# Kernel tuning notes

Measured on AMD Instinct MI355X. Metric: run time of the kernel, lower is better.

Reference implementation:

```python
import jax, jax.numpy as jnp
import numpy as np

FEATURE_MAPS = [38, 19, 10, 5, 3, 1]
NUM_ANCHORS = [4, 6, 6, 6, 4, 4]
SCALES = (0.2, 0.9)
RATIOS = np.array([1.0, 1.0, 2.0, 3.0, 0.5, 1.0 / 3.0])
BACKGROUND_ID = 0
EPS = 1e-6


def _generate_anchors():
    """Replicates AnchorManager._generate_anchors: order is (i, j, k)."""
    all_anchors = []
    for size, n in zip(FEATURE_MAPS, NUM_ANCHORS):
        scales = np.linspace(SCALES[0], SCALES[1], n)
        ratios = RATIOS[:n]
        rs = np.sqrt(ratios)
        w = scales * rs          # [n]
        h = scales / rs          # [n]
        cy = (np.arange(size) + 0.5) / size  # i -> rows (varies slowest)
        cx = (np.arange(size) + 0.5) / size  # j -> cols
        grid = np.zeros((size, size, n, 4), dtype=np.float64)
        grid[..., 0] = cx[None, :, None]
        grid[..., 1] = cy[:, None, None]
        grid[..., 2] = w[None, None, :]
        grid[..., 3] = h[None, None, :]
        all_anchors.append(grid.reshape(-1, 4))
    return np.concatenate(all_anchors).astype(np.float32)  # [A, 4] cxcywh


def _cxcywh_to_xyxy(b):
    cxy, wh = b[..., :2], b[..., 2:]
    return jnp.concatenate([cxy - wh / 2, cxy + wh / 2], axis=-1)


def _xyxy_to_cxcywh(b):
    xy1, xy2 = b[..., :2], b[..., 2:]
    return jnp.concatenate([(xy1 + xy2) / 2, xy2 - xy1], axis=-1)


def setup_inputs() -> dict:
    key = jax.random.key(0)
    k1, k2, k3 = jax.random.split(key, 3)
    B, N = 64, 100
    # valid normalized xyxy gt boxes
    xy = jax.random.uniform(k1, (B, N, 2), dtype=jnp.float32) * 0.8
    wh = jax.random.uniform(k2, (B, N, 2), dtype=jnp.float32) * 0.19 + 0.01
    gt_boxes = jnp.concatenate([xy, xy + wh], axis=-1)
    gt_labels = jax.random.randint(k3, (B, N), 1, 81, dtype=jnp.int64 if jax.config.jax_enable_x64 else jnp.int32).astype(jnp.int32)
    anchors_cxcywh = jnp.asarray(_generate_anchors())          # [A, 4]
    anchors_xyxy = _cxcywh_to_xyxy(anchors_cxcywh)             # [A, 4]
    return {
        "gt_labels": gt_labels,
        "gt_boxes": gt_boxes,
        "anchors_cxcywh": anchors_cxcywh,
        "anchors_xyxy": anchors_xyxy,
    }


def _iou(anchors_xyxy, gt_boxes):
    # anchors_xyxy: [A,4], gt_boxes: [B,N,4] -> iou [B,A,N]
    a = anchors_xyxy[None, :, None, :]   # [1,A,1,4]
    g = gt_boxes[:, None, :, :]          # [B,1,N,4]
    lt = jnp.maximum(a[..., :2], g[..., :2])
    rb = jnp.minimum(a[..., 2:], g[..., 2:])
    wh = jnp.clip(rb - lt, 0.0)
    inter = wh[..., 0] * wh[..., 1]
    area_a = (a[..., 2] - a[..., 0]) * (a[..., 3] - a[..., 1])
    area_g = (g[..., 2] - g[..., 0]) * (g[..., 3] - g[..., 1])
    return (inter / (area_a + area_g - inter)).astype(jnp.float32)


def reference(gt_labels, gt_boxes, anchors_cxcywh, anchors_xyxy):
    B, N = gt_boxes.shape[0], gt_boxes.shape[1]
    A = anchors_cxcywh.shape[0]

    gt_boxes_coco = _xyxy_to_cxcywh(gt_boxes)                  # [B,N,4]
    ious = _iou(anchors_xyxy, gt_boxes)                        # [B,A,N]

    anchors_gt = jnp.max(ious, axis=-1)                        # [B,A]
    anchors_gt_idx = jnp.argmax(ious, axis=-1)                 # [B,A]
    gt_anchors_idx = jnp.argmax(ious, axis=-2)                 # [B,N] best anchor per gt

    # force-match: each gt claims its best anchor
    b_idx = jnp.arange(B)[:, None]
    range_n = jnp.broadcast_to(jnp.arange(N), (B, N))
    anchors_gt_idx = anchors_gt_idx.at[b_idx, gt_anchors_idx].set(range_n)
    anchors_gt = anchors_gt.at[b_idx, gt_anchors_idx].set(2.0)

    pos_mask = anchors_gt > 0.5                                # [B,A]

    matched_gtb = jnp.take_along_axis(gt_boxes_coco, anchors_gt_idx[..., None], axis=1)  # [B,A,4]
    matched_labels = jnp.take_along_axis(gt_labels, anchors_gt_idx, axis=1)              # [B,A]
    encoded_labels = jnp.where(pos_mask, matched_labels, BACKGROUND_ID)

    anc = anchors_cxcywh[None]                                 # [1,A,4]
    enc_cxy = (matched_gtb[..., :2] - anc[..., :2]) / anc[..., 2:]
    enc_wh = jnp.log((matched_gtb[..., 2:] + EPS) / (anc[..., 2:] + EPS))
    encoded = jnp.concatenate([enc_cxy, enc_wh], axis=-1)      # [B,A,4]

    return encoded_labels, encoded, pos_mask
```

## Files before the change

### kernel.cpp

```cpp
#include <hip/hip_runtime.h>
#include <math.h>

#pragma clang fp contract(off)


#define AA 8732
#define NN 100
#define BB 64
#define EPS_F 1e-6f
#define OVR_FLAG 0x10000
#define DEFL 0.9999995f

__constant__ int FM_SIZE[6] = {38, 19, 10, 5, 3, 1};
__constant__ int FM_NF[6]   = {4, 6, 6, 6, 4, 4};
__constant__ int FM_OFF[6]  = {0, 5776, 7942, 8542, 8692, 8728};

__device__ __forceinline__ void geom(const float4 axy, const float4 g,
                                     float area_a, float ag,
                                     float& inter, float& uni) {
    float ltx = fmaxf(axy.x, g.x);
    float lty = fmaxf(axy.y, g.y);
    float rbx = fminf(axy.z, g.z);
    float rby = fminf(axy.w, g.w);
    float w = fmaxf(rbx - ltx, 0.0f);
    float h = fmaxf(rby - lty, 0.0f);
    inter = w * h;
    uni = area_a + ag - inter;
}

template <int N0, int N1>
__device__ __forceinline__ void phaseA(const float4 axy, float area_a,
                                       bool valid,
                                       const float4* sg, const float* sarea,
                                       const float* scurf,
                                       float& am, unsigned& rm, unsigned& cm) {
    #pragma unroll 4
    for (int n = N0; n < N1; n++) {
        float inter, uni;
        geom(axy, sg[n], area_a, sarea[n], inter, uni);
        float qa = inter * __builtin_amdgcn_rcpf(uni);
        bool r = (qa > 0.0f) && (qa >= am * DEFL);
        bool c = valid && (qa >= scurf[n]);
        am = fmaxf(am, qa);
        rm |= (r ? 1u : 0u) << (n - N0);
        cm |= (c ? 1u : 0u) << (n - N0);
    }
}

__global__ __launch_bounds__(256) void iou_pass_kernel(
        const float4* __restrict__ gt_boxes,
        const float4* __restrict__ anchors_xyxy,
        unsigned long long* __restrict__ colmax,
        float* __restrict__ out_val,
        int* __restrict__ out_slot)
{
    const int b = blockIdx.y;
    const int tid = threadIdx.x;
    const int a = blockIdx.x * 256 + tid;
    const bool valid = (a < AA);
    const int ac = valid ? a : (AA - 1);

    __shared__ float4 sg[NN];
    __shared__ float  sarea[NN];
    __shared__ float  scurf[NN];

    if (tid < NN) {
        float4 g = gt_boxes[b * NN + tid];
        sg[tid] = g;
        float ag = (g.z - g.x) * (g.w - g.y);
        sarea[tid] = ag;
        float cx = (g.x + g.z) * 0.5f;
        float cy = (g.y + g.w) * 0.5f;
        float best = 0.0f;
        for (int f = 0; f < 6; f++) {
            int s = FM_SIZE[f];
            int j = (int)(cx * (float)s); j = j < s - 1 ? j : s - 1;
            int i = (int)(cy * (float)s); i = i < s - 1 ? i : s - 1;
            int base = FM_OFF[f] + (i * s + j) * FM_NF[f];
            for (int k = 0; k < FM_NF[f]; k++) {
                float4 an = anchors_xyxy[base + k];
                float area_a = (an.z - an.x) * (an.w - an.y);
                float inter, uni;
                geom(an, g, area_a, ag, inter, uni);
                best = fmaxf(best, inter * __builtin_amdgcn_rcpf(uni));
            }
        }
        scurf[tid] = best * DEFL;
    }
    __syncthreads();

    const float4 axy = anchors_xyxy[ac];
    const float area_a = (axy.z - axy.x) * (axy.w - axy.y);

    float am = 0.0f;
    unsigned rm0 = 0, rm1 = 0, rm2 = 0, rm3 = 0;
    unsigned cm0 = 0, cm1 = 0, cm2 = 0, cm3 = 0;
    phaseA<0, 32>(axy, area_a, valid, sg, sarea, scurf, am, rm0, cm0);
    phaseA<32, 64>(axy, area_a, valid, sg, sarea, scurf, am, rm1, cm1);
    phaseA<64, 96>(axy, area_a, valid, sg, sarea, scurf, am, rm2, cm2);
    phaseA<96, NN>(axy, area_a, valid, sg, sarea, scurf, am, rm3, cm3);

    const float amthr = am * DEFL;
    float bv = 0.0f;
    int bi = 0;
    {
        unsigned rms[4] = {rm0, rm1, rm2, rm3};
        #pragma unroll
        for (int h = 0; h < 4; h++) {
            unsigned m = rms[h];
            const int nb = h * 32;
            while (m) {
                int n = __builtin_ctz(m) + nb;
                m &= m - 1;
                float inter, uni;
                geom(axy, sg[n], area_a, sarea[n], inter, uni);
                float qa = inter * __builtin_amdgcn_rcpf(uni);
                if (qa > 0.0f && qa >= amthr) {
                    float iou = inter / uni;
                    if (iou > bv) { bv = iou; bi = n; }
                }
            }
        }
    }

    {
        unsigned cms[4] = {cm0, cm1, cm2, cm3};
        #pragma unroll
        for (int h = 0; h < 4; h++) {
            unsigned wc = cms[h];
            #pragma unroll
            for (int off = 32; off > 0; off >>= 1)
                wc |= __shfl_xor(wc, off);
            const int nb = h * 32;
            while (wc) {
                int n = __builtin_ctz(wc) + nb;
                wc &= wc - 1;
                float inter, uni;
                geom(axy, sg[n], area_a, sarea[n], inter, uni);
                float qa = inter * __builtin_amdgcn_rcpf(uni);
                bool cc = valid && (qa >= scurf[n]);
                if (__any((int)cc)) {
                    float iou = inter / uni;
                    unsigned qb = cc ? __float_as_uint(iou) : 0u;
                    unsigned mm = qb;
                    #pragma unroll
                    for (int off = 32; off > 0; off >>= 1) {
                        unsigned o = __shfl_xor(mm, off);
                        mm = o > mm ? o : mm;
                    }
                    unsigned long long ball =
                        __ballot((int)(qb == mm && mm > 0u));
                    if (ball) {
                        int leader = __ffsll((long long)ball) - 1;
                        if ((tid & 63) == leader) {
                            unsigned long long v =
                                (((unsigned long long)mm) << 32) |
                                (unsigned long long)(unsigned)(AA - a);
                            atomicMax(colmax + b * NN + n, v);
                            atomicMax((unsigned*)&scurf[n],
                                __float_as_uint(__uint_as_float(mm) * DEFL));
                        }
                    }
                }
            }
        }
    }

    if (valid) {
        const size_t base = (size_t)b * AA + a;
        out_val[base] = bv;
        out_slot[base] = bi;
    }
}

__global__ void scatter_kernel(const unsigned long long* __restrict__ colmax,
                               int* __restrict__ out_slot) {
    const int b = blockIdx.x;
    const int n = threadIdx.x;
    if (n < NN) {
        unsigned long long v = colmax[b * NN + n];
        unsigned low = (unsigned)(v & 0xFFFFFFFFull);
        if (low >= 1u && low <= (unsigned)AA) {
            int idx = AA - (int)low;
            atomicMax(&out_slot[(size_t)b * AA + idx], OVR_FLAG + n);
        }
    }
}

__global__ __launch_bounds__(256) void encode_kernel(
        const int* __restrict__ gt_labels,
        const float4* __restrict__ gt_boxes,
        const float4* __restrict__ anchors_cxcywh,
        float* __restrict__ out)
{
    const int b = blockIdx.y;
    const int tid = threadIdx.x;
    const int a = blockIdx.x * 256 + tid;

    __shared__ float4 sg[NN];
    __shared__ int    slab[NN];
    if (tid < NN) {
        sg[tid]   = gt_boxes[b * NN + tid];
        slab[tid] = gt_labels[b * NN + tid];
    }
    __syncthreads();
    if (a >= AA) return;

    const size_t BA = (size_t)BB * AA;
    const size_t base = (size_t)b * AA + a;

    float bv = out[base];
    int s = ((const int*)(out + 5 * BA))[base];

    int idx; float val;
    if (s >= OVR_FLAG) { idx = s - OVR_FLAG; val = 2.0f; }
    else               { idx = s;            val = bv;   }
    const bool pos = val > 0.5f;

    const float4 g = sg[idx];
    const float gcx = (g.x + g.z) * 0.5f;
    const float gcy = (g.y + g.w) * 0.5f;
    const float gw  = g.z - g.x;
    const float gh  = g.w - g.y;

    const float4 anc = anchors_cxcywh[a];
    const float ecx = (gcx - anc.x) / anc.z;
    const float ecy = (gcy - anc.y) / anc.w;
    const float ew  = logf((gw + EPS_F) / (anc.z + EPS_F));
    const float eh  = logf((gh + EPS_F) / (anc.w + EPS_F));

    out[base] = pos ? (float)slab[idx] : 0.0f;
    ((float4*)(out + BA))[base] = make_float4(ecx, ecy, ew, eh);
    out[5 * BA + base] = pos ? 1.0f : 0.0f;
}

extern "C" void kernel_launch(void* const* d_in, const int* in_sizes, int n_in,
                              void* d_out, int out_size, void* d_ws, size_t ws_size,
                              hipStream_t stream) {
    const int*    gt_labels    = (const int*)d_in[0];
    const float4* gt_boxes     = (const float4*)d_in[1];
    const float4* anchors_cxcy = (const float4*)d_in[2];
    const float4* anchors_xyxy = (const float4*)d_in[3];
    float* out = (float*)d_out;

    const size_t BA = (size_t)BB * AA;
    unsigned long long* colmax = (unsigned long long*)(out + BA);
    int* slot = (int*)(out + 5 * BA);

    (void)hipMemsetAsync(colmax, 0,
                         (size_t)BB * NN * sizeof(unsigned long long), stream);

    dim3 grid((AA + 255) / 256, BB);
    iou_pass_kernel<<<grid, 256, 0, stream>>>(gt_boxes, anchors_xyxy, colmax,
                                              out, slot);
    scatter_kernel<<<BB, 128, 0, stream>>>(colmax, slot);
    encode_kernel<<<grid, 256, 0, stream>>>(gt_labels, gt_boxes, anchors_cxcy,
                                            out);
}
```

Measured before the change: 145.5 us.

## Process two anchors per thread and fuse column-max detection into main IoU loop

Each thread now handles two anchors, so every shared-memory ground-truth load is reused twice. The column-max update moves inline into the main loop through a 64-bit wave max reduction, which removes the second pass that recomputed IoU from per-thread column masks. The per-gt prior best-IoU computation moves to a separate small kernel that also initializes colmax, replacing the memset and the redundant per-block prior work. The trade-off is an extra launch, higher register pressure, half as many blocks, and an __any check on every iteration.

```diff
diff --git a/kernel.cpp b/kernel.cpp
--- a/kernel.cpp
+++ b/kernel.cpp
@@ -28,37 +28,129 @@
     uni = area_a + ag - inter;
 }
 
+__global__ void prior_kernel(const float4* __restrict__ gt_boxes,
+                             const float4* __restrict__ anchors_xyxy,
+                             float* __restrict__ prior,
+                             unsigned long long* __restrict__ colmax) {
+    const int b = blockIdx.x;
+    const int n = threadIdx.x;
+    if (n >= NN) return;
+    float4 g = gt_boxes[b * NN + n];
+    float ag = (g.z - g.x) * (g.w - g.y);
+    float cx = (g.x + g.z) * 0.5f;
+    float cy = (g.y + g.w) * 0.5f;
+    float best = 0.0f;
+    for (int f = 0; f < 6; f++) {
+        int s = FM_SIZE[f];
+        int j = (int)(cx * (float)s); j = j < s - 1 ? j : s - 1;
+        int i = (int)(cy * (float)s); i = i < s - 1 ? i : s - 1;
+        int base = FM_OFF[f] + (i * s + j) * FM_NF[f];
+        for (int k = 0; k < FM_NF[f]; k++) {
+            float4 an = anchors_xyxy[base + k];
+            float area_a = (an.z - an.x) * (an.w - an.y);
+            float inter, uni;
+            geom(an, g, area_a, ag, inter, uni);
+            best = fmaxf(best, inter * __builtin_amdgcn_rcpf(uni));
+        }
+    }
+    float defl = best * DEFL;
+    prior[b * NN + n] = defl;
+    colmax[b * NN + n] = ((unsigned long long)__float_as_uint(defl)) << 32;
+}
+
 template <int N0, int N1>
-__device__ __forceinline__ void phaseA(const float4 axy, float area_a,
-                                       bool valid,
-                                       const float4* sg, const float* sarea,
-                                       const float* scurf,
-                                       float& am, unsigned& rm, unsigned& cm) {
+__device__ __forceinline__ void passChunk(
+        const float4 x0, const float4 x1,
+        const float ar0, const float ar1,
+        const bool v0, const bool v1,
+        const int a0, const int a1,
+        const int b, const int tid,
+        const float4* __restrict__ sg,
+        const float* __restrict__ sarea,
+        float* scurf,
+        unsigned long long* __restrict__ colmax,
+        float& am0, float& am1,
+        unsigned& rm0, unsigned& rm1)
+{
     #pragma unroll 4
     for (int n = N0; n < N1; n++) {
-        float inter, uni;
-        geom(axy, sg[n], area_a, sarea[n], inter, uni);
-        float qa = inter * __builtin_amdgcn_rcpf(uni);
-        bool r = (qa > 0.0f) && (qa >= am * DEFL);
-        bool c = valid && (qa >= scurf[n]);
-        am = fmaxf(am, qa);
-        rm |= (r ? 1u : 0u) << (n - N0);
-        cm |= (c ? 1u : 0u) << (n - N0);
+        float4 g = sg[n];
+        float ag = sarea[n];
+        float i0, u0, i1, u1;
+        geom(x0, g, ar0, ag, i0, u0);
+        geom(x1, g, ar1, ag, i1, u1);
+        float q0 = i0 * __builtin_amdgcn_rcpf(u0);
+        float q1 = i1 * __builtin_amdgcn_rcpf(u1);
+        bool r0 = (q0 > 0.0f) && (q0 >= am0 * DEFL);
+        bool r1 = (q1 > 0.0f) && (q1 >= am1 * DEFL);
+        am0 = fmaxf(am0, q0);
+        am1 = fmaxf(am1, q1);
+        rm0 |= (r0 ? 1u : 0u) << (n - N0);
+        rm1 |= (r1 ? 1u : 0u) << (n - N0);
+        float cf = scurf[n];
+        bool c0 = v0 && (q0 >= cf);
+        bool c1 = v1 && (q1 >= cf);
+        if (__any((int)(c0 | c1))) {
+            float iou0 = i0 / u0;
+            float iou1 = i1 / u1;
+            unsigned long long p0 = c0
+                ? ((((unsigned long long)__float_as_uint(iou0)) << 32) |
+                   (unsigned long long)(unsigned)(AA - a0)) : 0ull;
+            unsigned long long p1 = c1
+                ? ((((unsigned long long)__float_as_uint(iou1)) << 32) |
+                   (unsigned long long)(unsigned)(AA - a1)) : 0ull;
+            unsigned long long p = p0 > p1 ? p0 : p1;
+            #pragma unroll
+            for (int off = 32; off > 0; off >>= 1) {
+                unsigned long long o = __shfl_xor(p, off);
+                p = o > p ? o : p;
+            }
+            if ((tid & 63) == 0 && p != 0ull) {
+                atomicMax(colmax + b * NN + n, p);
+                float nb = __uint_as_float((unsigned)(p >> 32)) * DEFL;
+                atomicMax((unsigned*)&scurf[n], __float_as_uint(nb));
+            }
+        }
+    }
+}
+
+__device__ __forceinline__ void rowScan(const float4 axy, const float area_a,
+        const float4* __restrict__ sg, const float* __restrict__ sarea,
+        const float amthr, const unsigned* rm, float& bv, int& bi)
+{
+    #pragma unroll
+    for (int h = 0; h < 4; h++) {
+        unsigned m = rm[h];
+        const int nb = h * 32;
+        while (m) {
+            int n = __builtin_ctz(m) + nb;
+            m &= m - 1;
+            float inter, uni;
+            geom(axy, sg[n], area_a, sarea[n], inter, uni);
+            float qa = inter * __builtin_amdgcn_rcpf(uni);
+            if (qa > 0.0f && qa >= amthr) {
+                float iou = inter / uni;
+                if (iou > bv) { bv = iou; bi = n; }
+            }
+        }
     }
 }
 
 __global__ __launch_bounds__(256) void iou_pass_kernel(
         const float4* __restrict__ gt_boxes,
         const float4* __restrict__ anchors_xyxy,
+        const float* __restrict__ prior,
         unsigned long long* __restrict__ colmax,
         float* __restrict__ out_val,
         int* __restrict__ out_slot)
 {
     const int b = blockIdx.y;
     const int tid = threadIdx.x;
-    const int a = blockIdx.x * 256 + tid;
-    const bool valid = (a < AA);
-    const int ac = valid ? a : (AA - 1);
+    const int a0 = blockIdx.x * 512 + tid;
+    const int a1 = a0 + 256;
+    const bool v0 = (a0 < AA), v1 = (a1 < AA);
+    const int ac0 = v0 ? a0 : (AA - 1);
+    const int ac1 = v1 ? a1 : (AA - 1);
 
     __shared__ float4 sg[NN];
     __shared__ float  sarea[NN];
@@ -67,109 +159,47 @@
     if (tid < NN) {
         float4 g = gt_boxes[b * NN + tid];
         sg[tid] = g;
-        float ag = (g.z - g.x) * (g.w - g.y);
-        sarea[tid] = ag;
-        float cx = (g.x + g.z) * 0.5f;
-        float cy = (g.y + g.w) * 0.5f;
-        float best = 0.0f;
-        for (int f = 0; f < 6; f++) {
-            int s = FM_SIZE[f];
-            int j = (int)(cx * (float)s); j = j < s - 1 ? j : s - 1;
-            int i = (int)(cy * (float)s); i = i < s - 1 ? i : s - 1;
-            int base = FM_OFF[f] + (i * s + j) * FM_NF[f];
-            for (int k = 0; k < FM_NF[f]; k++) {
-                float4 an = anchors_xyxy[base + k];
-                float area_a = (an.z - an.x) * (an.w - an.y);
-                float inter, uni;
-                geom(an, g, area_a, ag, inter, uni);
-                best = fmaxf(best, inter * __builtin_amdgcn_rcpf(uni));
-            }
-        }
-        scurf[tid] = best * DEFL;
+        sarea[tid] = (g.z - g.x) * (g.w - g.y);
+        scurf[tid] = prior[b * NN + tid];
     }
     __syncthreads();
 
-    const float4 axy = anchors_xyxy[ac];
-    const float area_a = (axy.z - axy.x) * (axy.w - axy.y);
-
-    float am = 0.0f;
-    unsigned rm0 = 0, rm1 = 0, rm2 = 0, rm3 = 0;
-    unsigned cm0 = 0, cm1 = 0, cm2 = 0, cm3 = 0;
-    phaseA<0, 32>(axy, area_a, valid, sg, sarea, scurf, am, rm0, cm0);
-    phaseA<32, 64>(axy, area_a, valid, sg, sarea, scurf, am, rm1, cm1);
-    phaseA<64, 96>(axy, area_a, valid, sg, sarea, scurf, am, rm2, cm2);
-    phaseA<96, NN>(axy, area_a, valid, sg, sarea, scurf, am, rm3, cm3);
-
-    const float amthr = am * DEFL;
-    float bv = 0.0f;
-    int bi = 0;
+    const float4 x0 = anchors_xyxy[ac0];
+    const float4 x1 = anchors_xyxy[ac1];
+    const float ar0 = (x0.z - x0.x) * (x0.w - x0.y);
+    const float ar1 = (x1.z - x1.x) * (x1.w - x1.y);
+
+    float am0 = 0.0f, am1 = 0.0f;
+    unsigned r0c0 = 0, r0c1 = 0, r0c2 = 0, r0c3 = 0;
+    unsigned r1c0 = 0, r1c1 = 0, r1c2 = 0, r1c3 = 0;
+    passChunk<0, 32>(x0, x1, ar0, ar1, v0, v1, a0, a1, b, tid,
+                     sg, sarea, scurf, colmax, am0, am1, r0c0, r1c0);
+    passChunk<32, 64>(x0, x1, ar0, ar1, v0, v1, a0, a1, b, tid,
+                      sg, sarea, scurf, colmax, am0, am1, r0c1, r1c1);
+    passChunk<64, 96>(x0, x1, ar0, ar1, v0, v1, a0, a1, b, tid,
+                      sg, sarea, scurf, colmax, am0, am1, r0c2, r1c2);
+    passChunk<96, NN>(x0, x1, ar0, ar1, v0, v1, a0, a1, b, tid,
+                      sg, sarea, scurf, colmax, am0, am1, r0c3, r1c3);
+
     {
-        unsigned rms[4] = {rm0, rm1, rm2, rm3};
-        #pragma unroll
-        for (int h = 0; h < 4; h++) {
-            unsigned m = rms[h];
-            const int nb = h * 32;
-            while (m) {
-                int n = __builtin_ctz(m) + nb;
-                m &= m - 1;
-                float inter, uni;
-                geom(axy, sg[n], area_a, sarea[n], inter, uni);
-                float qa = inter * __builtin_amdgcn_rcpf(uni);
-                if (qa > 0.0f && qa >= amthr) {
-                    float iou = inter / uni;
-                    if (iou > bv) { bv = iou; bi = n; }
-                }
-            }
-        }
-    }
-
+        unsigned rmA[4] = {r0c0, r0c1, r0c2, r0c3};
+        float bv = 0.0f; int bi = 0;
+        rowScan(x0, ar0, sg, sarea, am0 * DEFL, rmA, bv, bi);
+        if (v0) {
+            const size_t base = (size_t)b * AA + a0;
+            out_val[base] = bv;
+            out_slot[base] = bi;
+        }
+    }
     {
-        unsigned cms[4] = {cm0, cm1, cm2, cm3};
-        #pragma unroll
-        for (int h = 0; h < 4; h++) {
-            unsigned wc = cms[h];
-            #pragma unroll
-            for (int off = 32; off > 0; off >>= 1)
-                wc |= __shfl_xor(wc, off);
-            const int nb = h * 32;
-            while (wc) {
-                int n = __builtin_ctz(wc) + nb;
-                wc &= wc - 1;
-                float inter, uni;
-                geom(axy, sg[n], area_a, sarea[n], inter, uni);
-                float qa = inter * __builtin_amdgcn_rcpf(uni);
-                bool cc = valid && (qa >= scurf[n]);
-                if (__any((int)cc)) {
-                    float iou = inter / uni;
-                    unsigned qb = cc ? __float_as_uint(iou) : 0u;
-                    unsigned mm = qb;
-                    #pragma unroll
-                    for (int off = 32; off > 0; off >>= 1) {
-                        unsigned o = __shfl_xor(mm, off);
-                        mm = o > mm ? o : mm;
-                    }
-                    unsigned long long ball =
-                        __ballot((int)(qb == mm && mm > 0u));
-                    if (ball) {
-                        int leader = __ffsll((long long)ball) - 1;
-                        if ((tid & 63) == leader) {
-                            unsigned long long v =
-                                (((unsigned long long)mm) << 32) |
-                                (unsigned long long)(unsigned)(AA - a);
-                            atomicMax(colmax + b * NN + n, v);
-                            atomicMax((unsigned*)&scurf[n],
-                                __float_as_uint(__uint_as_float(mm) * DEFL));
-                        }
-                    }
-                }
-            }
-        }
-    }
-
-    if (valid) {
-        const size_t base = (size_t)b * AA + a;
-        out_val[base] = bv;
-        out_slot[base] = bi;
+        unsigned rmB[4] = {r1c0, r1c1, r1c2, r1c3};
+        float bv = 0.0f; int bi = 0;
+        rowScan(x1, ar1, sg, sarea, am1 * DEFL, rmB, bv, bi);
+        if (v1) {
+            const size_t base = (size_t)b * AA + a1;
+            out_val[base] = bv;
+            out_slot[base] = bi;
+        }
     }
 }
 
@@ -246,14 +276,16 @@
     const size_t BA = (size_t)BB * AA;
     unsigned long long* colmax = (unsigned long long*)(out + BA);
     int* slot = (int*)(out + 5 * BA);
-
-    (void)hipMemsetAsync(colmax, 0,
-                         (size_t)BB * NN * sizeof(unsigned long long), stream);
-
-    dim3 grid((AA + 255) / 256, BB);
-    iou_pass_kernel<<<grid, 256, 0, stream>>>(gt_boxes, anchors_xyxy, colmax,
-                                              out, slot);
+    float* prior = (float*)d_ws;
+
+    prior_kernel<<<BB, 128, 0, stream>>>(gt_boxes, anchors_xyxy, prior, colmax);
+
+    dim3 grid((AA + 511) / 512, BB);
+    iou_pass_kernel<<<grid, 256, 0, stream>>>(gt_boxes, anchors_xyxy, prior,
+                                              colmax, out, slot);
     scatter_kernel<<<BB, 128, 0, stream>>>(colmax, slot);
-    encode_kernel<<<grid, 256, 0, stream>>>(gt_labels, gt_boxes, anchors_cxcy,
-                                            out);
-}
+
+    dim3 grid2((AA + 255) / 256, BB);
+    encode_kernel<<<grid2, 256, 0, stream>>>(gt_labels, gt_boxes, anchors_cxcy,
+                                             out);
+}
```

New measurement: 142.6 us. 2.0% less time.

## Precompute per-GT prior IoU once and fuse column-max atomics into main loop

Applied to the files above, without the earlier changes.

Moves the per-GT best-nearby-anchor prior into a separate small kernel, so each block no longer recomputes it and colmax is seeded directly instead of memset. The column-max update is folded into the main IoU loop using a wave-wide 64-bit shuffle max plus atomics, removing the second pass over candidate masks. The positive flag is packed into the slot word so the float IoU value no longer has to be written and re-read. The trade-offs are an extra kernel launch, and a wave vote plus possible shuffle reduction on every iteration of the hot loop. Invalid lanes are also no longer excluded from the column candidates.

```diff
diff --git a/kernel.cpp b/kernel.cpp
--- a/kernel.cpp
+++ b/kernel.cpp
@@ -9,6 +9,7 @@
 #define BB 64
 #define EPS_F 1e-6f
 #define OVR_FLAG 0x10000
+#define POS_BIT  0x8000
 #define DEFL 0.9999995f
 
 __constant__ int FM_SIZE[6] = {38, 19, 10, 5, 3, 1};
@@ -28,30 +29,80 @@
     uni = area_a + ag - inter;
 }
 
+__global__ void prior_kernel(const float4* __restrict__ gt_boxes,
+                             const float4* __restrict__ anchors_xyxy,
+                             float* __restrict__ prior,
+                             unsigned long long* __restrict__ colmax) {
+    const int b = blockIdx.x;
+    const int n = threadIdx.x;
+    if (n >= NN) return;
+    float4 g = gt_boxes[b * NN + n];
+    float ag = (g.z - g.x) * (g.w - g.y);
+    float cx = (g.x + g.z) * 0.5f;
+    float cy = (g.y + g.w) * 0.5f;
+    float best = 0.0f;
+    for (int f = 0; f < 6; f++) {
+        int s = FM_SIZE[f];
+        int j = (int)(cx * (float)s); j = j < s - 1 ? j : s - 1;
+        int i = (int)(cy * (float)s); i = i < s - 1 ? i : s - 1;
+        int base = FM_OFF[f] + (i * s + j) * FM_NF[f];
+        for (int k = 0; k < FM_NF[f]; k++) {
+            float4 an = anchors_xyxy[base + k];
+            float area_a = (an.z - an.x) * (an.w - an.y);
+            float inter, uni;
+            geom(an, g, area_a, ag, inter, uni);
+            best = fmaxf(best, inter * __builtin_amdgcn_rcpf(uni));
+        }
+    }
+    float defl = best * DEFL;
+    prior[b * NN + n] = defl;
+    colmax[b * NN + n] = ((unsigned long long)__float_as_uint(defl)) << 32;
+}
+
 template <int N0, int N1>
-__device__ __forceinline__ void phaseA(const float4 axy, float area_a,
-                                       bool valid,
-                                       const float4* sg, const float* sarea,
-                                       const float* scurf,
-                                       float& am, unsigned& rm, unsigned& cm) {
+__device__ __forceinline__ void passChunk(
+        const float4 axy, const float area_a, const unsigned lowkey,
+        const int b, const int tid,
+        const float4* __restrict__ sg,
+        float2* sac,
+        unsigned long long* __restrict__ colmax,
+        float& rt, unsigned& rm)
+{
     #pragma unroll 4
     for (int n = N0; n < N1; n++) {
+        float4 g = sg[n];
+        float2 aw = sac[n];
         float inter, uni;
-        geom(axy, sg[n], area_a, sarea[n], inter, uni);
+        geom(axy, g, area_a, aw.x, inter, uni);
         float qa = inter * __builtin_amdgcn_rcpf(uni);
-        bool r = (qa > 0.0f) && (qa >= am * DEFL);
-        bool c = valid && (qa >= scurf[n]);
-        am = fmaxf(am, qa);
+        bool r = (qa > 0.0f) && (qa >= rt);
+        rt = fmaxf(rt, qa * DEFL);
         rm |= (r ? 1u : 0u) << (n - N0);
-        cm |= (c ? 1u : 0u) << (n - N0);
+        if (__any((int)(qa >= aw.y))) {
+            float iou = inter / uni;
+            bool cc = (qa >= aw.y);
+            unsigned long long p = cc
+                ? ((((unsigned long long)__float_as_uint(iou)) << 32) |
+                   (unsigned long long)lowkey) : 0ull;
+            #pragma unroll
+            for (int off = 32; off > 0; off >>= 1) {
+                unsigned long long o = __shfl_xor(p, off);
+                p = o > p ? o : p;
+            }
+            if ((tid & 63) == 0 && p != 0ull) {
+                atomicMax(colmax + b * NN + n, p);
+                atomicMax((unsigned*)&sac[n].y,
+                    __float_as_uint(__uint_as_float((unsigned)(p >> 32)) * DEFL));
+            }
+        }
     }
 }
 
 __global__ __launch_bounds__(256) void iou_pass_kernel(
         const float4* __restrict__ gt_boxes,
         const float4* __restrict__ anchors_xyxy,
+        const float* __restrict__ prior,
         unsigned long long* __restrict__ colmax,
-        float* __restrict__ out_val,
         int* __restrict__ out_slot)
 {
     const int b = blockIdx.y;
@@ -61,115 +112,49 @@
     const int ac = valid ? a : (AA - 1);
 
     __shared__ float4 sg[NN];
-    __shared__ float  sarea[NN];
-    __shared__ float  scurf[NN];
+    __shared__ float2 sac[NN];
 
     if (tid < NN) {
         float4 g = gt_boxes[b * NN + tid];
         sg[tid] = g;
-        float ag = (g.z - g.x) * (g.w - g.y);
-        sarea[tid] = ag;
-        float cx = (g.x + g.z) * 0.5f;
-        float cy = (g.y + g.w) * 0.5f;
-        float best = 0.0f;
-        for (int f = 0; f < 6; f++) {
-            int s = FM_SIZE[f];
-            int j = (int)(cx * (float)s); j = j < s - 1 ? j : s - 1;
-            int i = (int)(cy * (float)s); i = i < s - 1 ? i : s - 1;
-            int base = FM_OFF[f] + (i * s + j) * FM_NF[f];
-            for (int k = 0; k < FM_NF[f]; k++) {
-                float4 an = anchors_xyxy[base + k];
-                float area_a = (an.z - an.x) * (an.w - an.y);
-                float inter, uni;
-                geom(an, g, area_a, ag, inter, uni);
-                best = fmaxf(best, inter * __builtin_amdgcn_rcpf(uni));
-            }
-        }
-        scurf[tid] = best * DEFL;
+        sac[tid] = make_float2((g.z - g.x) * (g.w - g.y),
+                               prior[b * NN + tid]);
     }
     __syncthreads();
 
     const float4 axy = anchors_xyxy[ac];
     const float area_a = (axy.z - axy.x) * (axy.w - axy.y);
-
-    float am = 0.0f;
+    const unsigned lowkey = (unsigned)(AA - ac);
+
+    float rt = 0.0f;
     unsigned rm0 = 0, rm1 = 0, rm2 = 0, rm3 = 0;
-    unsigned cm0 = 0, cm1 = 0, cm2 = 0, cm3 = 0;
-    phaseA<0, 32>(axy, area_a, valid, sg, sarea, scurf, am, rm0, cm0);
-    phaseA<32, 64>(axy, area_a, valid, sg, sarea, scurf, am, rm1, cm1);
-    phaseA<64, 96>(axy, area_a, valid, sg, sarea, scurf, am, rm2, cm2);
-    phaseA<96, NN>(axy, area_a, valid, sg, sarea, scurf, am, rm3, cm3);
-
-    const float amthr = am * DEFL;
+    passChunk<0, 32>(axy, area_a, lowkey, b, tid, sg, sac, colmax, rt, rm0);
+    passChunk<32, 64>(axy, area_a, lowkey, b, tid, sg, sac, colmax, rt, rm1);
+    passChunk<64, 96>(axy, area_a, lowkey, b, tid, sg, sac, colmax, rt, rm2);
+    passChunk<96, NN>(axy, area_a, lowkey, b, tid, sg, sac, colmax, rt, rm3);
+
     float bv = 0.0f;
     int bi = 0;
-    {
-        unsigned rms[4] = {rm0, rm1, rm2, rm3};
-        #pragma unroll
-        for (int h = 0; h < 4; h++) {
-            unsigned m = rms[h];
-            const int nb = h * 32;
-            while (m) {
-                int n = __builtin_ctz(m) + nb;
-                m &= m - 1;
-                float inter, uni;
-                geom(axy, sg[n], area_a, sarea[n], inter, uni);
-                float qa = inter * __builtin_amdgcn_rcpf(uni);
-                if (qa > 0.0f && qa >= amthr) {
-                    float iou = inter / uni;
-                    if (iou > bv) { bv = iou; bi = n; }
-                }
+    unsigned rms[4] = {rm0, rm1, rm2, rm3};
+    #pragma unroll
+    for (int h = 0; h < 4; h++) {
+        unsigned m = rms[h];
+        const int nb = h * 32;
+        while (m) {
+            int n = __builtin_ctz(m) + nb;
+            m &= m - 1;
+            float inter, uni;
+            geom(axy, sg[n], area_a, sac[n].x, inter, uni);
+            float qa = inter * __builtin_amdgcn_rcpf(uni);
+            if (qa > 0.0f && qa >= rt) {
+                float iou = inter / uni;
+                if (iou > bv) { bv = iou; bi = n; }
             }
         }
     }
 
-    {
-        unsigned cms[4] = {cm0, cm1, cm2, cm3};
-        #pragma unroll
-        for (int h = 0; h < 4; h++) {
-            unsigned wc = cms[h];
-            #pragma unroll
-            for (int off = 32; off > 0; off >>= 1)
-                wc |= __shfl_xor(wc, off);
-            const int nb = h * 32;
-            while (wc) {
-                int n = __builtin_ctz(wc) + nb;
-                wc &= wc - 1;
-                float inter, uni;
-                geom(axy, sg[n], area_a, sarea[n], inter, uni);
-                float qa = inter * __builtin_amdgcn_rcpf(uni);
-                bool cc = valid && (qa >= scurf[n]);
-                if (__any((int)cc)) {
-                    float iou = inter / uni;
-                    unsigned qb = cc ? __float_as_uint(iou) : 0u;
-                    unsigned mm = qb;
-                    #pragma unroll
-                    for (int off = 32; off > 0; off >>= 1) {
-                        unsigned o = __shfl_xor(mm, off);
-                        mm = o > mm ? o : mm;
-                    }
-                    unsigned long long ball =
-                        __ballot((int)(qb == mm && mm > 0u));
-                    if (ball) {
-                        int leader = __ffsll((long long)ball) - 1;
-                        if ((tid & 63) == leader) {
-                            unsigned long long v =
-                                (((unsigned long long)mm) << 32) |
-                                (unsigned long long)(unsigned)(AA - a);
-                            atomicMax(colmax + b * NN + n, v);
-                            atomicMax((unsigned*)&scurf[n],
-                                __float_as_uint(__uint_as_float(mm) * DEFL));
-                        }
-                    }
-                }
-            }
-        }
-    }
-
     if (valid) {
-        const size_t base = (size_t)b * AA + a;
-        out_val[base] = bv;
-        out_slot[base] = bi;
+        out_slot[(size_t)b * AA + a] = bi | (bv > 0.5f ? POS_BIT : 0);
     }
 }
 
@@ -209,13 +194,11 @@
     const size_t BA = (size_t)BB * AA;
     const size_t base = (size_t)b * AA + a;
 
-    float bv = out[base];
     int s = ((const int*)(out + 5 * BA))[base];
 
-    int idx; float val;
-    if (s >= OVR_FLAG) { idx = s - OVR_FLAG; val = 2.0f; }
-    else               { idx = s;            val = bv;   }
-    const bool pos = val > 0.5f;
+    int idx; bool pos;
+    if (s >= OVR_FLAG) { idx = s - OVR_FLAG;  pos = true; }
+    else               { idx = s & 0x7FFF;    pos = (s & POS_BIT) != 0; }
 
     const float4 g = sg[idx];
     const float gcx = (g.x + g.z) * 0.5f;
@@ -246,13 +229,13 @@
     const size_t BA = (size_t)BB * AA;
     unsigned long long* colmax = (unsigned long long*)(out + BA);
     int* slot = (int*)(out + 5 * BA);
-
-    (void)hipMemsetAsync(colmax, 0,
-                         (size_t)BB * NN * sizeof(unsigned long long), stream);
+    float* prior = (float*)d_ws;
+
+    prior_kernel<<<BB, 128, 0, stream>>>(gt_boxes, anchors_xyxy, prior, colmax);
 
     dim3 grid((AA + 255) / 256, BB);
-    iou_pass_kernel<<<grid, 256, 0, stream>>>(gt_boxes, anchors_xyxy, colmax,
-                                              out, slot);
+    iou_pass_kernel<<<grid, 256, 0, stream>>>(gt_boxes, anchors_xyxy, prior,
+                                              colmax, slot);
     scatter_kernel<<<BB, 128, 0, stream>>>(colmax, slot);
     encode_kernel<<<grid, 256, 0, stream>>>(gt_labels, gt_boxes, anchors_cxcy,
                                             out);
```

Result: faster. 130.6 us (-10.3%).
